# Kernel tuning notes

Measured on AMD Instinct MI355X. Metric: run time of the kernel, lower is better.

## Reference

```python
import jax, jax.numpy as jnp
import numpy as np

# DCNv3 hyperparameters (from init_kwargs)
K = 3           # kernel_size
STRIDE = 1
PAD = 1
DIL = 1
GROUP = 4
GC = 16         # internelchannels = group_channels
CH = GROUP * GC # 64 internal channels
P = K * K       # sampling points per group
OFFSET_SCALE = 1.0


def setup_inputs() -> dict:
    key = jax.random.key(0)
    ks = jax.random.split(key, 8)
    B, H, W = 4, 128, 128
    cop_ch, aop_ch, out_ch = 64, 64, 64
    return {
        "x1": jax.random.normal(ks[0], (B, cop_ch, H, W), jnp.float32),
        "x2": jax.random.normal(ks[1], (B, aop_ch, H, W), jnp.float32),
        # value input projection (COP stream)
        "w_value": jax.random.normal(ks[2], (cop_ch, CH), jnp.float32) / np.sqrt(cop_ch),
        "b_value": jnp.zeros((CH,), jnp.float32),
        # offset/mask feature conv (AOP stream)
        "w_conv": jax.random.normal(ks[3], (K, K, aop_ch, CH), jnp.float32) / np.sqrt(K * K * aop_ch),
        "b_conv": jnp.zeros((CH,), jnp.float32),
        # offset head (small init so sampling stays near the regular grid)
        "w_offset": jax.random.normal(ks[4], (CH, GROUP * P * 2), jnp.float32) * 0.01,
        "b_offset": jnp.zeros((GROUP * P * 2,), jnp.float32),
        # mask head (softmax-normalized modulation)
        "w_mask": jax.random.normal(ks[5], (CH, GROUP * P), jnp.float32) * 0.1,
        "b_mask": jnp.zeros((GROUP * P,), jnp.float32),
        # output projection
        "w_out": jax.random.normal(ks[6], (CH, out_ch), jnp.float32) / np.sqrt(CH),
        "b_out": jnp.zeros((out_ch,), jnp.float32),
    }


def _bilinear_sample(vflat, x, y, Hp, Wp):
    """vflat: [B, Hp*Wp, G, gc]; x, y: [B, N, G] pixel coords in padded image.
    Returns [B, N, G, gc] zero-padded bilinear samples (grid_sample align_corners=False)."""
    x0 = jnp.floor(x)
    y0 = jnp.floor(y)
    out = jnp.zeros(vflat.shape[:1] + x.shape[1:] + vflat.shape[-1:], vflat.dtype)
    for dy in (0, 1):
        for dx in (0, 1):
            xi = x0 + dx
            yi = y0 + dy
            wgt = (1.0 - jnp.abs(x - xi)) * (1.0 - jnp.abs(y - yi))
            valid = (xi >= 0) & (xi < Wp) & (yi >= 0) & (yi < Hp)
            idx = (jnp.clip(yi, 0, Hp - 1) * Wp + jnp.clip(xi, 0, Wp - 1)).astype(jnp.int32)
            v = jnp.take_along_axis(vflat, idx[..., None], axis=1)  # [B,N,G,gc]
            out = out + v * (wgt * valid.astype(wgt.dtype))[..., None]
    return out


def reference(x1, x2, w_value, b_value, w_conv, b_conv,
              w_offset, b_offset, w_mask, b_mask, w_out, b_out):
    # NCHW -> NHWC (as in the torch wrapper)
    cop = jnp.transpose(x1, (0, 2, 3, 1))
    aop = jnp.transpose(x2, (0, 2, 3, 1))
    B, H, W, _ = cop.shape
    Hout = (H + 2 * PAD - DIL * (K - 1) - 1) // STRIDE + 1
    Wout = (W + 2 * PAD - DIL * (K - 1) - 1) // STRIDE + 1

    # value projection from COP stream: [B,H,W,CH]
    value = cop @ w_value + b_value

    # offset/mask branch from AOP stream
    feat = jax.lax.conv_general_dilated(
        aop, w_conv, (STRIDE, STRIDE), [(PAD, PAD), (PAD, PAD)],
        dimension_numbers=("NHWC", "HWIO", "NHWC")) + b_conv
    feat = jax.nn.gelu(feat)                                  # [B,Hout,Wout,CH]
    offset = (feat @ w_offset + b_offset).reshape(B, Hout, Wout, GROUP, P, 2)
    mask = jax.nn.softmax(
        (feat @ w_mask + b_mask).reshape(B, Hout, Wout, GROUP, P), axis=-1)

    # zero-pad the value map (DCNv3 pads input then samples in padded coords)
    vp = jnp.pad(value, ((0, 0), (PAD, PAD), (PAD, PAD), (0, 0)))
    Hp, Wp = H + 2 * PAD, W + 2 * PAD
    vflat = vp.reshape(B, Hp * Wp, GROUP, GC)

    # reference points + dilation grid (pixel coords in padded image)
    ref_x = (DIL * (K - 1) / 2 + jnp.arange(Wout, dtype=jnp.float32) * STRIDE)
    ref_y = (DIL * (K - 1) / 2 + jnp.arange(Hout, dtype=jnp.float32) * STRIDE)
    ky, kx = jnp.meshgrid(jnp.arange(K) - (K - 1) // 2,
                          jnp.arange(K) - (K - 1) // 2, indexing="ij")
    grid = jnp.stack([kx, ky], -1).reshape(P, 2).astype(jnp.float32) * DIL  # (dx,dy)

    x = (ref_x[None, None, :, None, None] + grid[None, None, None, None, :, 0]
         + offset[..., 0] * OFFSET_SCALE)                     # [B,Hout,Wout,G,P]
    y = (ref_y[None, :, None, None, None] + grid[None, None, None, None, :, 1]
         + offset[..., 1] * OFFSET_SCALE)

    # flatten to [B, N, G] with N = Hout*Wout*P (group axis kept last for gather)
    xr = jnp.transpose(x, (0, 1, 2, 4, 3)).reshape(B, Hout * Wout * P, GROUP)
    yr = jnp.transpose(y, (0, 1, 2, 4, 3)).reshape(B, Hout * Wout * P, GROUP)

    sampled = _bilinear_sample(vflat, xr, yr, Hp, Wp)         # [B,N,G,gc]
    sampled = sampled.reshape(B, Hout, Wout, P, GROUP, GC)

    out = jnp.einsum("bhwpgc,bhwgp->bhwgc", sampled, mask).reshape(B, Hout, Wout, CH)
    out = out @ w_out + b_out                                 # [B,Hout,Wout,out_ch]
    return jnp.transpose(out, (0, 3, 1, 2))                   # NHWC -> NCHW
```

## Files before the change

### kernel.cpp

```cpp
#include <hip/hip_runtime.h>
#include <cstdint>
#include <cstddef>

typedef float f4 __attribute__((ext_vector_type(4)));
typedef float f2 __attribute__((ext_vector_type(2)));
typedef float f32x4 __attribute__((ext_vector_type(4)));
typedef short short8 __attribute__((ext_vector_type(8)));
typedef unsigned int u32;
typedef unsigned short u16;
typedef u32 u32x2 __attribute__((ext_vector_type(2)));
typedef u32 u32x4 __attribute__((ext_vector_type(4)));


__device__ __forceinline__ u16 f2bf(float f) {
    u32 u = __builtin_bit_cast(u32, f);
    return (u16)((u + 0x7FFFu + ((u >> 16) & 1u)) >> 16);
}

__device__ __forceinline__ int xcd_swz10(int d) {
    return ((d & 7) << 7) | (d >> 3);
}
__device__ __forceinline__ int xcd_swz11(int d) {
    return ((d & 7) << 8) | (d >> 3);
}

__global__ __launch_bounds__(256, 4) void mega_prep_k(float* __restrict__ vpad,
                                                      char* __restrict__ x2tp,
                                                      const float* __restrict__ wc,
                                                      const float* __restrict__ wo,
                                                      const float* __restrict__ wm,
                                                      char* __restrict__ wbfT,
                                                      char* __restrict__ whead,
                                                      const float* __restrict__ x2,
                                                      const float* __restrict__ x1,
                                                      const float* __restrict__ wv,
                                                      const float* __restrict__ bv) {
    __shared__ __align__(16) char smem[32768];
    int blk = blockIdx.x;

    if (blk < 425) {
        if (blk < 260) {
            int i = blk * 256 + threadIdx.x;
            if (i >= 66560) return;
            int c4 = i & 15;
            int rest = i >> 4;
            int b = rest / 1040;
            int e = rest - b * 1040;
            int y, x;
            if (e < 132)      { y = 0;   x = e; }
            else if (e < 264) { y = 1;   x = e - 132; }
            else if (e < 396) { y = 130; x = e - 264; }
            else if (e < 528) { y = 131; x = e - 396; }
            else { int e2 = e - 528; y = 2 + (e2 >> 2); int m = e2 & 3;
                   x = (m < 2) ? m : m + 128; }
            f4 z = {0.f, 0.f, 0.f, 0.f};
            *(f4*)(vpad + (((size_t)b * 17424 + (size_t)y * 132 + x) * 64 + c4 * 4)) = z;
        } else if (blk < 325) {
            int i = (blk - 260) * 256 + threadIdx.x;
            if (i >= 16512) return;
            int c8 = i & 7;
            int rest = i >> 3;
            int b = rest / 516;
            int e = rest - b * 516;
            int y, x;
            if (e < 130)      { y = 0;       x = e; }
            else if (e < 260) { y = 129;     x = e - 130; }
            else if (e < 388) { y = e - 259; x = 0; }
            else              { y = e - 387; x = 129; }
            u32x4 z = {0u, 0u, 0u, 0u};
            *(u32x4*)(x2tp + ((size_t)b * 16900 + (size_t)y * 130 + x) * 128 + c8 * 16) = z;
        } else if (blk < 397) {
            int i = (blk - 325) * 256 + threadIdx.x;
            int c = i / 288, kp = i - c * 288;
            int k = kp << 1;
            float f0 = wc[(size_t)k * 64 + c];
            float f1 = wc[(size_t)(k + 1) * 64 + c];
            u32 pk = (u32)f2bf(f0) | ((u32)f2bf(f1) << 16);
            *(u32*)(wbfT + (size_t)c * 1152 + kp * 4) = pk;
        } else {
            int i = (blk - 397) * 256 + threadIdx.x;
            int k = i & 63, col = i >> 6;
            float v = 0.f;
            if (col < 72)       v = wo[(size_t)k * 72 + col];
            else if (col < 108) v = wm[(size_t)k * 36 + col - 72];
            *(u16*)(whead + (size_t)(col * 64 + k) * 2) = f2bf(v);
        }
    } else if (blk < 937) {
        u32* tr = (u32*)smem;
        int local = blk - 425;
        int t = threadIdx.x;
        int y = local & 127, b = local >> 7;
        const float* xb = x2 + (size_t)b * 64 * 16384 + (size_t)y * 128;
        #pragma unroll 4
        for (int j = 0; j < 16; j++) {
            int idx = t + (j << 8);
            int x = idx & 127, cip = idx >> 7;
            int ci = cip << 1;
            float f0 = xb[(size_t)ci * 16384 + x];
            float f1 = xb[(size_t)(ci + 1) * 16384 + x];
            u32 pk = (u32)f2bf(f0) | ((u32)f2bf(f1) << 16);
            int key = (x + 1) & 7;
            int byt = x * 128 + (((ci >> 3) ^ key) << 4) + (ci & 7) * 2;
            tr[byt >> 2] = pk;
        }
        __syncthreads();
        const u32x4* src = (const u32x4*)tr;
        u32x4* dst = (u32x4*)(x2tp + ((size_t)(b * 130 + y + 1) * 130 + 1) * 128);
        #pragma unroll
        for (int j = 0; j < 4; j++) {
            int c = t + (j << 8);
            dst[c] = src[c];
        }
    } else {
        float (*xs)[64]  = (float(*)[64])smem;
        float (*wsh)[64] = (float(*)[64])(smem + 16384);
        int tid = threadIdx.x;
        int bidx = xcd_swz10(blk - 937);
        int xb = bidx & 1;
        int y  = (bidx >> 1) & 127;
        int b  = bidx >> 8;
        int x0 = xb * 64;

        #pragma unroll
        for (int j = 0; j < 4; j++) {
            int chunk = tid + j * 256;
            int ci = chunk >> 4, p4 = chunk & 15;
            *(f4*)&xs[ci][p4 * 4] =
                *(const f4*)(x1 + (((size_t)b * 64 + ci) * 128 + y) * 128 + x0 + p4 * 4);
            *(f4*)&wsh[ci][p4 * 4] = *(const f4*)(wv + ci * 64 + p4 * 4);
        }
        __syncthreads();

        int c0 = (tid & 15) * 4, p0 = (tid >> 4) * 4;
        f4 bb = *(const f4*)(bv + c0);
        f4 acc[4];
        #pragma unroll
        for (int i = 0; i < 4; i++) acc[i] = bb;

        #pragma unroll
        for (int ci = 0; ci < 64; ci++) {
            f4 w4 = *(f4*)&wsh[ci][c0];
            f4 x4 = *(f4*)&xs[ci][p0];
            #pragma unroll
            for (int i = 0; i < 4; i++) acc[i] += x4[i] * w4;
        }

        #pragma unroll
        for (int i = 0; i < 4; i++) {
            int xp = x0 + p0 + i + 2;
            *(f4*)(vpad + (((size_t)b * 132 + (y + 2)) * 132 + xp) * 64 + c0) = acc[i];
        }
    }
}

__global__ __launch_bounds__(128, 4) void conv_mfma_k(const char* __restrict__ x2tp,
                                                      const char* __restrict__ wbfT,
                                                      const float* __restrict__ bc,
                                                      char* __restrict__ featb) {
    __shared__ char slab[3 * 4352];
    int tid = threadIdx.x;
    int l = tid & 63, w = tid >> 6;
    int bidx = xcd_swz11(blockIdx.x);
    int xq = bidx & 3, y = (bidx >> 2) & 127, b = bidx >> 9;
    int x0 = xq << 5;

    const char* gr = x2tp + ((size_t)(b * 130 + y) * 130 + x0) * 128;
    for (int q = tid; q < 816; q += 128) {
        int r = q / 272, c = q - r * 272;
        const char* g = gr + (size_t)r * (130 * 128) + c * 16;
        char* p = slab + q * 16;
        __builtin_amdgcn_global_load_lds(
            (const __attribute__((address_space(1))) u32*)g,
            (__attribute__((address_space(3))) u32*)p, 16, 0, 0);
    }
    __syncthreads();

    int m0 = w << 4;
    int r16 = l & 15, g16 = l >> 4;
    f32x4 acc[4] = {{0.f,0.f,0.f,0.f},{0.f,0.f,0.f,0.f},
                    {0.f,0.f,0.f,0.f},{0.f,0.f,0.f,0.f}};
    const char* wb = wbfT + (size_t)r16 * 1152 + g16 * 16;

    #pragma unroll
    for (int s = 0; s < 18; s++) {
        const int t9 = s >> 1;
        const int ky = t9 / 3, kx = t9 - ky * 3;
        const int ci0g = (s & 1) * 4;
        int x_sl = m0 + r16 + kx;
        int go = (ci0g + g16) ^ (x_sl & 7);
        short8 a = *(const short8*)(slab + ky * 4352 + x_sl * 128 + go * 16);
        #pragma unroll
        for (int cb = 0; cb < 4; cb++) {
            short8 bf = *(const short8*)(wb + (size_t)cb * (16 * 1152) + s * 64);
            acc[cb] = __builtin_amdgcn_mfma_f32_16x16x32_bf16(bf, a, acc[cb], 0, 0, 0);
        }
    }

    const float kA = 0.7978845608028654f, kB = 0.044715f;
    char* fp = featb + ((size_t)b * 16384 + (size_t)y * 128 + x0 + m0 + r16) * 128;
    #pragma unroll
    for (int cb = 0; cb < 4; cb++) {
        f4 b4 = *(const f4*)(bc + cb * 16 + g16 * 4);
        u16 h[4];
        #pragma unroll
        for (int j = 0; j < 4; j++) {
            float v = acc[cb][j] + b4[j];
            float z = kA * (v + kB * v * v * v);
            float e = __expf(2.f * z);
            float th = 1.f - 2.f / (e + 1.f);
            h[j] = f2bf(0.5f * v * (1.f + th));
        }
        u32x2 pk = {(u32)h[0] | ((u32)h[1] << 16), (u32)h[2] | ((u32)h[3] << 16)};
        *(u32x2*)(fp + cb * 32 + g16 * 8) = pk;
    }
}

__global__ __launch_bounds__(256, 6) void dcn_fused_v5(const char* __restrict__ featb,
                                                       const float* __restrict__ vpad,
                                                       const char* __restrict__ whead,
                                                       const float* __restrict__ bo,
                                                       const float* __restrict__ bm,
                                                       const float* __restrict__ wout,
                                                       const float* __restrict__ bout,
                                                       float* __restrict__ out) {
    __shared__ float off_s [4][8][74];
    __shared__ float msk_s [4][8][38];
    __shared__ float samp_s[4][8][64];

    int tid = threadIdx.x;
    int w = tid >> 6, l = tid & 63;
    int blk = xcd_swz11(blockIdx.x);
    int b = blk >> 9, y = (blk >> 2) & 127, xq = blk & 3;
    int x0w = xq * 32 + w * 8;
    int pix0 = ((b << 7) + y) * 128 + x0w;

    int r = l & 15, q = l >> 4;

    const char* fpt = featb + (size_t)(pix0 + (r & 7)) * 128 + q * 16;
    short8 a0 = *(const short8*)fpt;
    short8 a1 = *(const short8*)(fpt + 64);

    const char* wh = whead + (size_t)r * 128 + q * 16;
    f32x4 hc[7];
    #pragma unroll
    for (int t = 0; t < 7; t++) {
        short8 b0 = *(const short8*)(wh + t * 2048);
        short8 b1 = *(const short8*)(wh + t * 2048 + 64);
        f32x4 z = {0.f, 0.f, 0.f, 0.f};
        z = __builtin_amdgcn_mfma_f32_16x16x32_bf16(a0, b0, z, 0, 0, 0);
        hc[t] = __builtin_amdgcn_mfma_f32_16x16x32_bf16(a1, b1, z, 0, 0, 0);
    }

    if (q < 2) {
        #pragma unroll
        for (int t = 0; t < 7; t++) {
            int col = t * 16 + r;
            float bias = 0.f;
            if (col < 72)        bias = bo[col];
            else if (col < 108)  bias = bm[col - 72];
            #pragma unroll
            for (int j = 0; j < 4; j++) {
                int px = q * 4 + j;
                float v = hc[t][j] + bias;
                if (col < 72)       off_s[w][px][col] = v;
                else if (col < 108) msk_s[w][px][col - 72] = v;
            }
        }
    }

    if (l < 32) {
        int px = l >> 2, g = l & 3;
        float m[9];
        #pragma unroll
        for (int p = 0; p < 9; p++) m[p] = msk_s[w][px][g * 9 + p];
        float mx = m[0];
        #pragma unroll
        for (int p = 1; p < 9; p++) mx = fmaxf(mx, m[p]);
        float s = 0.f;
        #pragma unroll
        for (int p = 0; p < 9; p++) { m[p] = __expf(m[p] - mx); s += m[p]; }
        float inv = 1.f / s;
        #pragma unroll
        for (int p = 0; p < 9; p++) msk_s[w][px][g * 9 + p] = m[p] * inv;
    }

    {
        int cc4 = l & 3, g = (l >> 2) & 3, pxs = l >> 4;
        const float* vb = vpad + (size_t)b * 17424 * 64 + g * 16 + cc4 * 4;
        #pragma unroll
        for (int j = 0; j < 2; j++) {
            int px = pxs * 2 + j;
            int xpix = x0w + px;
            f4 acc = {0.f, 0.f, 0.f, 0.f};
            #pragma unroll
            for (int p = 0; p < 9; p++) {
                const int kx = p % 3, ky = p / 3;
                f2 oxy = *(const f2*)&off_s[w][px][g * 18 + 2 * p];
                float mv = msk_s[w][px][g * 9 + p];
                float sx = (float)(xpix + kx) + oxy[0];
                float sy = (float)(y + ky) + oxy[1];
                float xf = floorf(sx), yf = floorf(sy);
                float fx = sx - xf, fy = sy - yf;
                int ix = (int)xf, iy = (int)yf;
                int e0 = (iy * 132 + ix + 133) << 6;
                const float* pa = vb + e0;
                f4 v00 = *(const f4*)pa;
                f4 v01 = *(const f4*)(pa + 64);
                f4 v10 = *(const f4*)(pa + 8448);
                f4 v11 = *(const f4*)(pa + 8512);
                float wy0 = mv * (1.f - fy), wy1 = mv * fy;
                float w00 = wy0 * (1.f - fx), w01 = wy0 * fx;
                float w10 = wy1 * (1.f - fx), w11 = wy1 * fx;
                #pragma unroll
                for (int c = 0; c < 4; c++)
                    acc[c] = fmaf(w00, v00[c],
                             fmaf(w01, v01[c],
                             fmaf(w10, v10[c],
                             fmaf(w11, v11[c], acc[c]))));
            }
            *(f4*)&samp_s[w][px][g * 16 + cc4 * 4] = acc;
        }
    }

    float oa[8];
    float bvv = bout[l];
    #pragma unroll
    for (int px = 0; px < 8; px++) oa[px] = bvv;
    const float* pw = wout + l;
    #pragma unroll 4
    for (int k4 = 0; k4 < 16; k4++) {
        float w0 = pw[0], w1 = pw[64], w2 = pw[128], w3 = pw[192];
        pw += 256;
        #pragma unroll
        for (int px = 0; px < 8; px++) {
            f4 sv = *(f4*)&samp_s[w][px][k4 * 4];
            oa[px] = fmaf(sv[0], w0, fmaf(sv[1], w1,
                     fmaf(sv[2], w2, fmaf(sv[3], w3, oa[px]))));
        }
    }

    float* op = out + ((size_t)b * 64 + l) * 16384 + y * 128 + x0w;
    f4 o0 = {oa[0], oa[1], oa[2], oa[3]};
    f4 o1 = {oa[4], oa[5], oa[6], oa[7]};
    *(f4*)op       = o0;
    *(f4*)(op + 4) = o1;
}

extern "C" void kernel_launch(void* const* d_in, const int* in_sizes, int n_in,
                              void* d_out, int out_size, void* d_ws, size_t ws_size,
                              hipStream_t stream) {
    const float* x1       = (const float*)d_in[0];
    const float* x2       = (const float*)d_in[1];
    const float* w_value  = (const float*)d_in[2];
    const float* b_value  = (const float*)d_in[3];
    const float* w_conv   = (const float*)d_in[4];
    const float* b_conv   = (const float*)d_in[5];
    const float* w_offset = (const float*)d_in[6];
    const float* b_offset = (const float*)d_in[7];
    const float* w_mask   = (const float*)d_in[8];
    const float* b_mask   = (const float*)d_in[9];
    const float* w_out    = (const float*)d_in[10];
    const float* b_out    = (const float*)d_in[11];

    float* vpad  = (float*)d_ws;
    char*  featb = (char*)d_ws + 17842176;
    char*  x2tp  = (char*)d_ws + 26230784;
    char*  wbfT  = (char*)d_ws + 34883584;
    char*  whead = (char*)d_ws + 34957312;
    float* outp  = (float*)d_out;

    hipLaunchKernelGGL(mega_prep_k,  dim3(1961), dim3(256), 0, stream,
                       vpad, x2tp, w_conv, w_offset, w_mask, wbfT, whead,
                       x2, x1, w_value, b_value);
    hipLaunchKernelGGL(conv_mfma_k,  dim3(2048), dim3(128), 0, stream,
                       x2tp, wbfT, b_conv, featb);
    hipLaunchKernelGGL(dcn_fused_v5, dim3(2048), dim3(256), 0, stream,
                       featb, vpad, whead, b_offset, b_mask, w_out, b_out, outp);
}
```

Before: 192.2 us.

## Fuse offset-feature conv into the DCN kernel, keeping features in LDS

Merges the MFMA 3x3 conv+GELU kernel with the deformable sampling kernel into one 256-thread kernel. Each block now computes its 32-pixel bf16 feature tile into shared memory and consumes it directly for the offset/mask heads. This removes the global featb round trip and one kernel launch. Shared memory is overlaid: the input slab region is reused for offsets and masks after a barrier. The conv work is split across four waves (two pixel halves by two channel-block pairs), and the fused kernel's register and LDS footprint may lower occupancy.

Result: faster. 185.8 us (-3.3%).

```diff
diff --git a/kernel.cpp b/kernel.cpp
--- a/kernel.cpp
+++ b/kernel.cpp
@@ -153,21 +153,34 @@
     }
 }
 
-__global__ __launch_bounds__(128, 4) void conv_mfma_k(const char* __restrict__ x2tp,
-                                                      const char* __restrict__ wbfT,
-                                                      const float* __restrict__ bc,
-                                                      char* __restrict__ featb) {
-    __shared__ char slab[3 * 4352];
+__global__ __launch_bounds__(256, 6) void conv_dcn_k(const char* __restrict__ x2tp,
+                                                     const char* __restrict__ wbfT,
+                                                     const float* __restrict__ bc,
+                                                     const float* __restrict__ vpad,
+                                                     const char* __restrict__ whead,
+                                                     const float* __restrict__ bo,
+                                                     const float* __restrict__ bm,
+                                                     const float* __restrict__ wout,
+                                                     const float* __restrict__ bout,
+                                                     float* __restrict__ out) {
+    __shared__ __align__(16) char smem[26624];
+    char*  slab  = smem;
+    float* off_s = (float*)smem;
+    float* msk_s = (float*)(smem + 9472);
+    char*  featl = smem + 14336;
+    float* samp_s= (float*)(smem + 18432);
+
     int tid = threadIdx.x;
     int l = tid & 63, w = tid >> 6;
-    int bidx = xcd_swz11(blockIdx.x);
-    int xq = bidx & 3, y = (bidx >> 2) & 127, b = bidx >> 9;
+    int blk = xcd_swz11(blockIdx.x);
+    int b = blk >> 9, y = (blk >> 2) & 127, xq = blk & 3;
     int x0 = xq << 5;
+    int r16 = l & 15, g16 = l >> 4;
 
     const char* gr = x2tp + ((size_t)(b * 130 + y) * 130 + x0) * 128;
-    for (int q = tid; q < 816; q += 128) {
-        int r = q / 272, c = q - r * 272;
-        const char* g = gr + (size_t)r * (130 * 128) + c * 16;
+    for (int q = tid; q < 816; q += 256) {
+        int rr = q / 272, c = q - rr * 272;
+        const char* g = gr + (size_t)rr * (130 * 128) + c * 16;
         char* p = slab + q * 16;
         __builtin_amdgcn_global_load_lds(
             (const __attribute__((address_space(1))) u32*)g,
@@ -175,68 +188,52 @@
     }
     __syncthreads();
 
-    int m0 = w << 4;
-    int r16 = l & 15, g16 = l >> 4;
-    f32x4 acc[4] = {{0.f,0.f,0.f,0.f},{0.f,0.f,0.f,0.f},
-                    {0.f,0.f,0.f,0.f},{0.f,0.f,0.f,0.f}};
-    const char* wb = wbfT + (size_t)r16 * 1152 + g16 * 16;
-
-    #pragma unroll
-    for (int s = 0; s < 18; s++) {
-        const int t9 = s >> 1;
-        const int ky = t9 / 3, kx = t9 - ky * 3;
-        const int ci0g = (s & 1) * 4;
-        int x_sl = m0 + r16 + kx;
-        int go = (ci0g + g16) ^ (x_sl & 7);
-        short8 a = *(const short8*)(slab + ky * 4352 + x_sl * 128 + go * 16);
-        #pragma unroll
-        for (int cb = 0; cb < 4; cb++) {
-            short8 bf = *(const short8*)(wb + (size_t)cb * (16 * 1152) + s * 64);
-            acc[cb] = __builtin_amdgcn_mfma_f32_16x16x32_bf16(bf, a, acc[cb], 0, 0, 0);
-        }
-    }
-
-    const float kA = 0.7978845608028654f, kB = 0.044715f;
-    char* fp = featb + ((size_t)b * 16384 + (size_t)y * 128 + x0 + m0 + r16) * 128;
-    #pragma unroll
-    for (int cb = 0; cb < 4; cb++) {
-        f4 b4 = *(const f4*)(bc + cb * 16 + g16 * 4);
-        u16 h[4];
-        #pragma unroll
-        for (int j = 0; j < 4; j++) {
-            float v = acc[cb][j] + b4[j];
-            float z = kA * (v + kB * v * v * v);
-            float e = __expf(2.f * z);
-            float th = 1.f - 2.f / (e + 1.f);
-            h[j] = f2bf(0.5f * v * (1.f + th));
-        }
-        u32x2 pk = {(u32)h[0] | ((u32)h[1] << 16), (u32)h[2] | ((u32)h[3] << 16)};
-        *(u32x2*)(fp + cb * 32 + g16 * 8) = pk;
-    }
-}
-
-__global__ __launch_bounds__(256, 6) void dcn_fused_v5(const char* __restrict__ featb,
-                                                       const float* __restrict__ vpad,
-                                                       const char* __restrict__ whead,
-                                                       const float* __restrict__ bo,
-                                                       const float* __restrict__ bm,
-                                                       const float* __restrict__ wout,
-                                                       const float* __restrict__ bout,
-                                                       float* __restrict__ out) {
-    __shared__ float off_s [4][8][74];
-    __shared__ float msk_s [4][8][38];
-    __shared__ float samp_s[4][8][64];
-
-    int tid = threadIdx.x;
-    int w = tid >> 6, l = tid & 63;
-    int blk = xcd_swz11(blockIdx.x);
-    int b = blk >> 9, y = (blk >> 2) & 127, xq = blk & 3;
-    int x0w = xq * 32 + w * 8;
-    int pix0 = ((b << 7) + y) * 128 + x0w;
-
-    int r = l & 15, q = l >> 4;
-
-    const char* fpt = featb + (size_t)(pix0 + (r & 7)) * 128 + q * 16;
+    {
+        int m0c = (w & 1) << 4;
+        int cbb = (w >> 1) << 1;
+        f32x4 acc[2] = {{0.f,0.f,0.f,0.f},{0.f,0.f,0.f,0.f}};
+        const char* wb = wbfT + (size_t)r16 * 1152 + g16 * 16;
+
+        #pragma unroll
+        for (int s = 0; s < 18; s++) {
+            const int t9 = s >> 1;
+            const int ky = t9 / 3, kx = t9 - ky * 3;
+            const int ci0g = (s & 1) * 4;
+            int x_sl = m0c + r16 + kx;
+            int go = (ci0g + g16) ^ (x_sl & 7);
+            short8 a = *(const short8*)(slab + ky * 4352 + x_sl * 128 + go * 16);
+            #pragma unroll
+            for (int c2 = 0; c2 < 2; c2++) {
+                short8 bf = *(const short8*)(wb + (size_t)(cbb + c2) * 18432 + s * 64);
+                acc[c2] = __builtin_amdgcn_mfma_f32_16x16x32_bf16(bf, a, acc[c2], 0, 0, 0);
+            }
+        }
+
+        const float kA = 0.7978845608028654f, kB = 0.044715f;
+        char* fp = featl + (size_t)(m0c + r16) * 128;
+        #pragma unroll
+        for (int c2 = 0; c2 < 2; c2++) {
+            int cb = cbb + c2;
+            f4 b4 = *(const f4*)(bc + cb * 16 + g16 * 4);
+            u16 h[4];
+            #pragma unroll
+            for (int j = 0; j < 4; j++) {
+                float v = acc[c2][j] + b4[j];
+                float z = kA * (v + kB * v * v * v);
+                float e = __expf(2.f * z);
+                float th = 1.f - 2.f / (e + 1.f);
+                h[j] = f2bf(0.5f * v * (1.f + th));
+            }
+            u32x2 pk = {(u32)h[0] | ((u32)h[1] << 16), (u32)h[2] | ((u32)h[3] << 16)};
+            *(u32x2*)(fp + cb * 32 + g16 * 8) = pk;
+        }
+    }
+    __syncthreads();
+
+    int x0w = x0 + w * 8;
+    int r = r16, q = g16;
+
+    const char* fpt = featl + (size_t)(w * 8 + (r & 7)) * 128 + q * 16;
     short8 a0 = *(const short8*)fpt;
     short8 a1 = *(const short8*)(fpt + 64);
 
@@ -262,17 +259,18 @@
             for (int j = 0; j < 4; j++) {
                 int px = q * 4 + j;
                 float v = hc[t][j] + bias;
-                if (col < 72)       off_s[w][px][col] = v;
-                else if (col < 108) msk_s[w][px][col - 72] = v;
+                if (col < 72)       off_s[(w * 8 + px) * 74 + col] = v;
+                else if (col < 108) msk_s[(w * 8 + px) * 38 + (col - 72)] = v;
             }
         }
     }
 
     if (l < 32) {
         int px = l >> 2, g = l & 3;
+        float* m9 = &msk_s[(w * 8 + px) * 38 + g * 9];
         float m[9];
         #pragma unroll
-        for (int p = 0; p < 9; p++) m[p] = msk_s[w][px][g * 9 + p];
+        for (int p = 0; p < 9; p++) m[p] = m9[p];
         float mx = m[0];
         #pragma unroll
         for (int p = 1; p < 9; p++) mx = fmaxf(mx, m[p]);
@@ -281,7 +279,7 @@
         for (int p = 0; p < 9; p++) { m[p] = __expf(m[p] - mx); s += m[p]; }
         float inv = 1.f / s;
         #pragma unroll
-        for (int p = 0; p < 9; p++) msk_s[w][px][g * 9 + p] = m[p] * inv;
+        for (int p = 0; p < 9; p++) m9[p] = m[p] * inv;
     }
 
     {
@@ -291,12 +289,14 @@
         for (int j = 0; j < 2; j++) {
             int px = pxs * 2 + j;
             int xpix = x0w + px;
+            const float* offp = &off_s[(w * 8 + px) * 74 + g * 18];
+            const float* mskp = &msk_s[(w * 8 + px) * 38 + g * 9];
             f4 acc = {0.f, 0.f, 0.f, 0.f};
             #pragma unroll
             for (int p = 0; p < 9; p++) {
                 const int kx = p % 3, ky = p / 3;
-                f2 oxy = *(const f2*)&off_s[w][px][g * 18 + 2 * p];
-                float mv = msk_s[w][px][g * 9 + p];
+                f2 oxy = *(const f2*)&offp[2 * p];
+                float mv = mskp[p];
                 float sx = (float)(xpix + kx) + oxy[0];
                 float sy = (float)(y + ky) + oxy[1];
                 float xf = floorf(sx), yf = floorf(sy);
@@ -318,7 +318,7 @@
                              fmaf(w10, v10[c],
                              fmaf(w11, v11[c], acc[c]))));
             }
-            *(f4*)&samp_s[w][px][g * 16 + cc4 * 4] = acc;
+            *(f4*)&samp_s[(w * 8 + px) * 64 + g * 16 + cc4 * 4] = acc;
         }
     }
 
@@ -333,7 +333,7 @@
         pw += 256;
         #pragma unroll
         for (int px = 0; px < 8; px++) {
-            f4 sv = *(f4*)&samp_s[w][px][k4 * 4];
+            f4 sv = *(f4*)&samp_s[(w * 8 + px) * 64 + k4 * 4];
             oa[px] = fmaf(sv[0], w0, fmaf(sv[1], w1,
                      fmaf(sv[2], w2, fmaf(sv[3], w3, oa[px]))));
         }
@@ -363,17 +363,15 @@
     const float* b_out    = (const float*)d_in[11];
 
     float* vpad  = (float*)d_ws;
-    char*  featb = (char*)d_ws + 17842176;
-    char*  x2tp  = (char*)d_ws + 26230784;
-    char*  wbfT  = (char*)d_ws + 34883584;
-    char*  whead = (char*)d_ws + 34957312;
+    char*  x2tp  = (char*)d_ws + 17842176;
+    char*  wbfT  = (char*)d_ws + 26494976;
+    char*  whead = (char*)d_ws + 26568704;
     float* outp  = (float*)d_out;
 
-    hipLaunchKernelGGL(mega_prep_k,  dim3(1961), dim3(256), 0, stream,
+    hipLaunchKernelGGL(mega_prep_k, dim3(1961), dim3(256), 0, stream,
                        vpad, x2tp, w_conv, w_offset, w_mask, wbfT, whead,
                        x2, x1, w_value, b_value);
-    hipLaunchKernelGGL(conv_mfma_k,  dim3(2048), dim3(128), 0, stream,
-                       x2tp, wbfT, b_conv, featb);
-    hipLaunchKernelGGL(dcn_fused_v5, dim3(2048), dim3(256), 0, stream,
-                       featb, vpad, whead, b_offset, b_mask, w_out, b_out, outp);
-}
+    hipLaunchKernelGGL(conv_dcn_k,  dim3(2048), dim3(256), 0, stream,
+                       x2tp, wbfT, b_conv, vpad, whead,
+                       b_offset, b_mask, w_out, b_out, outp);
+}
```
